# Optimization experiments

Measured on AMD Instinct MI355X. Metric: run time of the kernel, lower is better.

The kernel has to match this reference:

```python
import jax, jax.numpy as jnp
import numpy as np


def _flip_neg(a):
    # index k -> a[(-k) mod n] along last axis (torch.roll(torch.flip(a,-1),1,-1))
    return jnp.roll(jnp.flip(a, axis=-1), 1, axis=-1)


def setup_inputs() -> dict:
    key = jax.random.key(0)
    k1, k2 = jax.random.split(key)
    B, C, L, M = 16, 64, 65536, 512
    x = jax.random.normal(k1, (B, C, L), dtype=jnp.float32)
    scale = 1.0 / (C * C)
    weights1 = scale * jax.random.uniform(k2, (C, C, M), dtype=jnp.float32)
    return {"x": x, "weights1": weights1}


def reference(x, weights1):
    B, Cin, L = x.shape
    M = weights1.shape[-1]
    two_pi = jnp.asarray(2.0 * np.pi, dtype=x.dtype)

    # pseudo-DHT: elementwise modulation along length
    k = jnp.arange(L, dtype=x.dtype)
    theta = two_pi * k / L
    x_ht = x * (jnp.cos(theta) - jnp.sin(theta))  # (B, Cin, L)

    # mode-limited channel mixing (compl_mul1d)
    x1 = x_ht[:, :, :M]                 # (B, Cin, M)
    x1n = _flip_neg(x1)
    wn = _flip_neg(weights1)
    out_m = 0.5 * (
        jnp.einsum('bix,iox->box', x1, weights1)
        - jnp.einsum('bix,iox->box', x1n, wn)
        + jnp.einsum('bix,iox->box', x1, wn)
        + jnp.einsum('bix,iox->box', x1n, weights1)
    )  # (B, Cout, M)

    # zero-init half-spectrum buffer, slice-assign low modes
    Lh = L // 2 + 1
    Cout = weights1.shape[1]
    out = jnp.zeros((B, Cout, Lh), dtype=x.dtype).at[:, :, :M].set(out_m)

    # idht: same pseudo-DHT on the (B, Cout, Lh) buffer, normalized by size(1)=channels
    k2 = jnp.arange(Lh, dtype=x.dtype)
    theta2 = two_pi * k2 / Lh
    out = out * (jnp.cos(theta2) - jnp.sin(theta2)) / Cin
    return out
```

## Files before the change

### kernel.cpp

```cpp
#include <hip/hip_runtime.h>
#include <math.h>

#define B_   16
#define CIN  64
#define COUT 64
#define L_   65536
#define M_   512
#define LH_  32769

#define NBLK     2048
#define NTHREADS (NBLK * 256)
#define N4       ((B_ * COUT * LH_) / 4)

__global__ __launch_bounds__(256) void fused_spectral(
    const float* __restrict__ x, const float* __restrict__ w, float* __restrict__ out)
{
    __shared__ float4 red[256];

    const int wv   = (int)threadIdx.x >> 6;
    const int lane = (int)threadIdx.x & 63;
    const int cw   = (int)blockIdx.x;

    const int m  = ((cw & 7) << 6) + lane;
    const int o0 = ((cw >> 3) & 31) * 2;
    const int b0 = (cw >> 8) * 2;
    const int m2 = (M_ - m) & (M_ - 1);

    float a00 = 0.f, a01 = 0.f, a10 = 0.f, a11 = 0.f;
    {
        const float TWO_PI = 6.28318530717958647692f;
        const float t1  = TWO_PI * (float)m  / (float)L_;
        const float t1n = TWO_PI * (float)m2 / (float)L_;
        const float c1m = cosf(t1)  - sinf(t1);
        const float c1n = cosf(t1n) - sinf(t1n);

        const float* xA = x + (size_t)b0 * CIN * L_;
        const float* xB = xA + (size_t)CIN * L_;
        const int i0 = wv * 16;

        #pragma unroll 4
        for (int ii = 0; ii < 16; ++ii) {
            const size_t ro = (size_t)(i0 + ii) * L_;
            const float xmA = xA[ro + m]  * c1m;
            const float xnA = xA[ro + m2] * c1n;
            const float xmB = xB[ro + m]  * c1m;
            const float xnB = xB[ro + m2] * c1n;

            const float* wr = w + (size_t)((i0 + ii) * COUT + o0) * M_;
            const float wm0 = wr[m],      wn0 = wr[m2];
            const float wm1 = wr[M_ + m], wn1 = wr[M_ + m2];
            const float ws0 = wm0 + wn0, wd0 = wm0 - wn0;
            const float ws1 = wm1 + wn1, wd1 = wm1 - wn1;

            a00 += xmA * ws0 + xnA * wd0;
            a01 += xmA * ws1 + xnA * wd1;
            a10 += xmB * ws0 + xnB * wd0;
            a11 += xmB * ws1 + xnB * wd1;
        }
    }

    red[threadIdx.x] = make_float4(a00, a01, a10, a11);
    __syncthreads();

    if (wv == 0) {
        const float4 r0 = red[lane];
        const float4 r1 = red[64 + lane];
        const float4 r2 = red[128 + lane];
        const float4 r3 = red[192 + lane];
        const float TWO_PI = 6.28318530717958647692f;
        const float t2 = TWO_PI * (float)m / (float)LH_;
        const float c2 = (cosf(t2) - sinf(t2)) * (0.5f / (float)CIN);
        out[(size_t)((b0 + 0) * COUT + o0 + 0) * LH_ + m] = c2 * (r0.x + r1.x + r2.x + r3.x);
        out[(size_t)((b0 + 0) * COUT + o0 + 1) * LH_ + m] = c2 * (r0.y + r1.y + r2.y + r3.y);
        out[(size_t)((b0 + 1) * COUT + o0 + 0) * LH_ + m] = c2 * (r0.z + r1.z + r2.z + r3.z);
        out[(size_t)((b0 + 1) * COUT + o0 + 1) * LH_ + m] = c2 * (r0.w + r1.w + r2.w + r3.w);
    }

    const int tid = cw * 256 + (int)threadIdx.x;
    for (int j = tid; j < N4; j += NTHREADS) {
        const unsigned flat = (unsigned)j * 4u;
        const unsigned row  = flat / (unsigned)LH_;
        const unsigned col  = flat - row * (unsigned)LH_;
        if (col >= (unsigned)M_ && col <= (unsigned)(LH_ - 4)) {
            const float4 z = {0.f, 0.f, 0.f, 0.f};
            reinterpret_cast<float4*>(out)[j] = z;
        } else {
            #pragma unroll
            for (int e = 0; e < 4; ++e) {
                const unsigned f   = flat + (unsigned)e;
                const unsigned r2_ = f / (unsigned)LH_;
                const unsigned c2_ = f - r2_ * (unsigned)LH_;
                if (c2_ >= (unsigned)M_) out[f] = 0.f;
            }
        }
    }
}

extern "C" void kernel_launch(void* const* d_in, const int* in_sizes, int n_in,
                              void* d_out, int out_size, void* d_ws, size_t ws_size,
                              hipStream_t stream) {
    const float* x = (const float*)d_in[0];
    const float* w = (const float*)d_in[1];
    float* out = (float*)d_out;

    fused_spectral<<<NBLK, 256, 0, stream>>>(x, w, out);
}
```

Baseline: 38.93 us.

## Enlarge register tile to 4 batches by 4 outputs per block and spread reduction

Each block now computes a 4x4 tile of (batch, output channel) per mode instead of 2x2. This cuts the grid from 2048 to 512 blocks and reuses each loaded x and weight value across more accumulators, lowering redundant global loads. The cross-wave reduction is spread over all four waves through a padded shared array rather than done by wave 0 alone. In exchange, fewer blocks also handle the large zero-fill of the output, so each thread does more of that store loop, and register pressure rises.

```diff
diff --git a/kernel.cpp b/kernel.cpp
--- a/kernel.cpp
+++ b/kernel.cpp
@@ -8,25 +8,27 @@
 #define M_   512
 #define LH_  32769
 
-#define NBLK     2048
+#define NBLK     512
 #define NTHREADS (NBLK * 256)
 #define N4       ((B_ * COUT * LH_) / 4)
 
 __global__ __launch_bounds__(256) void fused_spectral(
     const float* __restrict__ x, const float* __restrict__ w, float* __restrict__ out)
 {
-    __shared__ float4 red[256];
+    __shared__ float red[256][17];
 
     const int wv   = (int)threadIdx.x >> 6;
     const int lane = (int)threadIdx.x & 63;
     const int cw   = (int)blockIdx.x;
 
     const int m  = ((cw & 7) << 6) + lane;
-    const int o0 = ((cw >> 3) & 31) * 2;
-    const int b0 = (cw >> 8) * 2;
+    const int o0 = ((cw >> 3) & 15) * 4;
+    const int b0 = (cw >> 7) * 4;
     const int m2 = (M_ - m) & (M_ - 1);
 
-    float a00 = 0.f, a01 = 0.f, a10 = 0.f, a11 = 0.f;
+    float acc[16];
+    #pragma unroll
+    for (int k = 0; k < 16; ++k) acc[k] = 0.f;
     {
         const float TWO_PI = 6.28318530717958647692f;
         const float t1  = TWO_PI * (float)m  / (float)L_;
@@ -34,46 +36,45 @@
         const float c1m = cosf(t1)  - sinf(t1);
         const float c1n = cosf(t1n) - sinf(t1n);
 
-        const float* xA = x + (size_t)b0 * CIN * L_;
-        const float* xB = xA + (size_t)CIN * L_;
         const int i0 = wv * 16;
-
-        #pragma unroll 4
+        #pragma unroll 2
         for (int ii = 0; ii < 16; ++ii) {
-            const size_t ro = (size_t)(i0 + ii) * L_;
-            const float xmA = xA[ro + m]  * c1m;
-            const float xnA = xA[ro + m2] * c1n;
-            const float xmB = xB[ro + m]  * c1m;
-            const float xnB = xB[ro + m2] * c1n;
-
-            const float* wr = w + (size_t)((i0 + ii) * COUT + o0) * M_;
-            const float wm0 = wr[m],      wn0 = wr[m2];
-            const float wm1 = wr[M_ + m], wn1 = wr[M_ + m2];
-            const float ws0 = wm0 + wn0, wd0 = wm0 - wn0;
-            const float ws1 = wm1 + wn1, wd1 = wm1 - wn1;
-
-            a00 += xmA * ws0 + xnA * wd0;
-            a01 += xmA * ws1 + xnA * wd1;
-            a10 += xmB * ws0 + xnB * wd0;
-            a11 += xmB * ws1 + xnB * wd1;
+            const int i = i0 + ii;
+            float xm[4], xn[4];
+            #pragma unroll
+            for (int bb = 0; bb < 4; ++bb) {
+                const float* xr = x + ((size_t)(b0 + bb) * CIN + i) * L_;
+                xm[bb] = xr[m]  * c1m;
+                xn[bb] = xr[m2] * c1n;
+            }
+            const float* wi = w + ((size_t)i * COUT + o0) * M_;
+            #pragma unroll
+            for (int oo = 0; oo < 4; ++oo) {
+                const float wm = wi[(size_t)oo * M_ + m];
+                const float wn = wi[(size_t)oo * M_ + m2];
+                const float ws = wm + wn, wd = wm - wn;
+                #pragma unroll
+                for (int bb = 0; bb < 4; ++bb)
+                    acc[bb * 4 + oo] += xm[bb] * ws + xn[bb] * wd;
+            }
         }
     }
 
-    red[threadIdx.x] = make_float4(a00, a01, a10, a11);
+    #pragma unroll
+    for (int k = 0; k < 16; ++k) red[threadIdx.x][k] = acc[k];
     __syncthreads();
 
-    if (wv == 0) {
-        const float4 r0 = red[lane];
-        const float4 r1 = red[64 + lane];
-        const float4 r2 = red[128 + lane];
-        const float4 r3 = red[192 + lane];
+    {
         const float TWO_PI = 6.28318530717958647692f;
         const float t2 = TWO_PI * (float)m / (float)LH_;
         const float c2 = (cosf(t2) - sinf(t2)) * (0.5f / (float)CIN);
-        out[(size_t)((b0 + 0) * COUT + o0 + 0) * LH_ + m] = c2 * (r0.x + r1.x + r2.x + r3.x);
-        out[(size_t)((b0 + 0) * COUT + o0 + 1) * LH_ + m] = c2 * (r0.y + r1.y + r2.y + r3.y);
-        out[(size_t)((b0 + 1) * COUT + o0 + 0) * LH_ + m] = c2 * (r0.z + r1.z + r2.z + r3.z);
-        out[(size_t)((b0 + 1) * COUT + o0 + 1) * LH_ + m] = c2 * (r0.w + r1.w + r2.w + r3.w);
+        #pragma unroll
+        for (int k = 0; k < 4; ++k) {
+            const int a = wv * 4 + k;
+            const float s = red[lane][a] + red[64 + lane][a]
+                          + red[128 + lane][a] + red[192 + lane][a];
+            out[(size_t)((b0 + wv) * COUT + o0 + k) * LH_ + m] = c2 * s;
+        }
     }
 
     const int tid = cw * 256 + (int)threadIdx.x;
```

New measurement: 51.10 us. +31.2%, slower.
